# Optimization experiments

Measured on AMD Instinct MI355X. Metric: run time of the kernel, lower is better.

## Reference

```python
import jax, jax.numpy as jnp
import numpy as np

MODES = (16, 16)

def setup_inputs() -> dict:
    key = jax.random.key(0)
    ks = jax.random.split(key, 8)
    B, Cin, Cout, H, W = 16, 64, 64, 128, 128
    scale = 1.0 / (Cin * Cout)
    return {
        "x": jax.random.normal(ks[0], (B, Cin, H, W), jnp.float32),
        "t_emb": jax.random.normal(ks[1], (B, 512), jnp.float32),
        "weight_real": jax.random.normal(ks[2], (Cin, Cout, *MODES), jnp.float32) * 2 * scale - scale,
        "weight_imag": jax.random.normal(ks[3], (Cin, Cout, *MODES), jnp.float32) * 2 * scale - scale,
        "bypass_w": jax.random.normal(ks[4], (Cout, Cin), jnp.float32) * 0.05,
        "bypass_b": jax.random.normal(ks[5], (Cout,), jnp.float32) * 0.05,
        "temb_w": jax.random.normal(ks[6], (Cin, 512), jnp.float32) * 0.02,
        "temb_b": jax.random.normal(ks[7], (Cin,), jnp.float32) * 0.02,
    }

def reference(x, t_emb, weight_real, weight_imag, bypass_w, bypass_b, temb_w, temb_b):
    mk, ml = MODES
    H, W = x.shape[-2:]
    xf = x.astype(jnp.float32)
    # truncated spectral conv: rfft2 (ortho), keep low-mode corner only
    x_fft = jnp.fft.rfftn(xf, axes=(-2, -1), norm="ortho")[:, :, :mk, :ml]
    weight = weight_real + 1j * weight_imag  # [i, o, k, l]
    out_fft = jnp.einsum("bikl,iokl->bokl", x_fft, weight)
    x_spec = jnp.fft.irfftn(out_fft, s=(H, W), axes=(-2, -1), norm="ortho")
    # 1x1 conv bypass
    byp = jnp.einsum("bihw,oi->bohw", xf, bypass_w) + bypass_b[None, :, None, None]
    out = jax.nn.gelu(x_spec + byp, approximate=False)
    # temb fusion: x + Linear(silu(temb))[:, :, None, None]
    silu_t = t_emb * jax.nn.sigmoid(t_emb)
    proj = silu_t @ temb_w.T + temb_b  # [B, C]
    out = out + proj[:, :, None, None]
    return out
```

## Files before the change

kernel.cpp:

```cpp
#include <hip/hip_runtime.h>
#include <cmath>

#define TWO_PI_128 0.04908738521234052f

typedef __attribute__((ext_vector_type(8))) short bf16x8;
typedef __attribute__((ext_vector_type(4))) float f32x4;

__device__ inline unsigned short f2bf(float v) {
  unsigned u = __float_as_uint(v);
  unsigned r = (u + 0x7FFFu + ((u >> 16) & 1u)) >> 16;
  return (unsigned short)r;
}

__global__ __launch_bounds__(256) void front_kernel(
    const float* __restrict__ x, float* __restrict__ xfr_t,
    float* __restrict__ xfi_t, const float* __restrict__ wr,
    const float* __restrict__ wi, float* __restrict__ wt_r,
    float* __restrict__ wt_i, const float* __restrict__ t_emb,
    const float* __restrict__ temb_w, const float* __restrict__ temb_b,
    float* __restrict__ proj) {
  __shared__ union SM {
    struct {
      unsigned short x1[32 * 136];
      float red[8 * 256];
    } f;
    float tile[32][33];
    struct {
      float silu[512];
      float part[64][4];
    } p;
  } sm;

  const int bid = blockIdx.x;
  const int t = threadIdx.x;

  if (bid >= 3072) {
    const int b = bid - 3072;
    for (int j = t; j < 512; j += 256) {
      float v = t_emb[b * 512 + j];
      sm.p.silu[j] = v / (1.f + __expf(-v));
    }
    __syncthreads();
    const int o = t >> 2, part = t & 3;
    const float* wrow = temb_w + o * 512 + part * 128;
    const float* srow = sm.p.silu + part * 128;
    float acc = 0.f;
#pragma unroll 8
    for (int j = 0; j < 128; ++j) acc = fmaf(srow[j], wrow[j], acc);
    sm.p.part[o][part] = acc;
    __syncthreads();
    if (part == 0) {
      proj[b * 64 + o] = sm.p.part[o][0] + sm.p.part[o][1] + sm.p.part[o][2] +
                         sm.p.part[o][3] + temb_b[o];
    }
    return;
  }

  if (bid >= 1024) {
    const int flat = bid - 1024;
    const int tensor = flat >> 10;
    const int rem = flat & 1023;
    const int io0 = (rem >> 3) * 32, kl0 = (rem & 7) * 32;
    const float* src = tensor ? wi : wr;
    float* dst = tensor ? wt_i : wt_r;
    const int ty = t >> 3, tx = t & 7;
    float4 v = *(const float4*)(src + (size_t)(io0 + ty) * 256 + kl0 + 4 * tx);
    sm.tile[ty][4 * tx + 0] = v.x;
    sm.tile[ty][4 * tx + 1] = v.y;
    sm.tile[ty][4 * tx + 2] = v.z;
    sm.tile[ty][4 * tx + 3] = v.w;
    __syncthreads();
    float4 o;
    o.x = sm.tile[4 * tx + 0][ty];
    o.y = sm.tile[4 * tx + 1][ty];
    o.z = sm.tile[4 * tx + 2][ty];
    o.w = sm.tile[4 * tx + 3][ty];
    *(float4*)(dst + (size_t)(kl0 + ty) * 4096 + io0 + 4 * tx) = o;
    return;
  }

  const int plane = bid;
  const int wv = t >> 6, lane = t & 63, l15 = lane & 15, quad = lane >> 4;

  union U8 {
    bf16x8 v;
    unsigned short u[8];
  };

  float dC, dS;
  sincosf(TWO_PI_128 * (float)l15, &dS, &dC);

  U8 a_re[4], a_im[4];
#pragma unroll
  for (int ks = 0; ks < 4; ++ks) {
    const int w0 = ks * 32 + quad * 8;
    float c, s;
    sincosf(TWO_PI_128 * (float)((l15 * w0) & 127), &s, &c);
#pragma unroll
    for (int j = 0; j < 8; ++j) {
      a_re[ks].u[j] = f2bf(c);
      a_im[ks].u[j] = f2bf(-s);
      float nc = c * dC - s * dS;
      s = s * dC + c * dS;
      c = nc;
    }
  }

  const float* xp = x + (size_t)plane * 16384;
  f32x4 acc[2][2];
#pragma unroll
  for (int mt = 0; mt < 2; ++mt)
#pragma unroll
    for (int nt = 0; nt < 2; ++nt) acc[mt][nt] = (f32x4){0.f, 0.f, 0.f, 0.f};

#pragma unroll
  for (int ks = 0; ks < 4; ++ks) {
#pragma unroll
    for (int nt = 0; nt < 2; ++nt) {
      const float* src =
          xp + (size_t)((wv * 2 + nt) * 16 + l15) * 128 + ks * 32 + quad * 8;
      float4 v0 = *(const float4*)src;
      float4 v1 = *(const float4*)(src + 4);
      U8 bx;
      bx.u[0] = f2bf(v0.x);
      bx.u[1] = f2bf(v0.y);
      bx.u[2] = f2bf(v0.z);
      bx.u[3] = f2bf(v0.w);
      bx.u[4] = f2bf(v1.x);
      bx.u[5] = f2bf(v1.y);
      bx.u[6] = f2bf(v1.z);
      bx.u[7] = f2bf(v1.w);
      acc[0][nt] = __builtin_amdgcn_mfma_f32_16x16x32_bf16(a_re[ks].v, bx.v,
                                                           acc[0][nt], 0, 0, 0);
      acc[1][nt] = __builtin_amdgcn_mfma_f32_16x16x32_bf16(a_im[ks].v, bx.v,
                                                           acc[1][nt], 0, 0, 0);
    }
  }

#pragma unroll
  for (int mt = 0; mt < 2; ++mt)
#pragma unroll
    for (int nt = 0; nt < 2; ++nt)
#pragma unroll
      for (int r = 0; r < 4; ++r)
        sm.f.x1[(mt * 16 + quad * 4 + r) * 136 + (wv * 2 + nt) * 16 + l15] =
            f2bf(acc[mt][nt][r]);
  __syncthreads();

  f32x4 accre = (f32x4){0.f, 0.f, 0.f, 0.f};
  f32x4 accim = (f32x4){0.f, 0.f, 0.f, 0.f};
#pragma unroll
  for (int kl2 = 0; kl2 < 2; ++kl2) {
    const int ks2 = wv * 2 + kl2;
    const int hb = (ks2 & 3) * 32 + quad * 8;
    const int imh = ks2 >> 2;
    float c, s;
    sincosf(TWO_PI_128 * (float)((l15 * hb) & 127), &s, &c);
    U8 ar, ai;
#pragma unroll
    for (int j = 0; j < 8; ++j) {
      if (!imh) {
        ar.u[j] = f2bf(c);
        ai.u[j] = f2bf(-s);
      } else {
        ar.u[j] = f2bf(s);
        ai.u[j] = f2bf(c);
      }
      float nc = c * dC - s * dS;
      s = s * dC + c * dS;
      c = nc;
    }
    bf16x8 bfrag = *(const bf16x8*)(sm.f.x1 + (imh * 16 + l15) * 136 + hb);
    accre =
        __builtin_amdgcn_mfma_f32_16x16x32_bf16(ar.v, bfrag, accre, 0, 0, 0);
    accim =
        __builtin_amdgcn_mfma_f32_16x16x32_bf16(ai.v, bfrag, accim, 0, 0, 0);
  }
  *(f32x4*)(sm.f.red + (wv * 2) * 256 + lane * 4) = accre;
  *(f32x4*)(sm.f.red + (wv * 2 + 1) * 256 + lane * 4) = accim;
  __syncthreads();

  const float re =
      sm.f.red[t] + sm.f.red[512 + t] + sm.f.red[1024 + t] + sm.f.red[1536 + t];
  const float im = sm.f.red[256 + t] + sm.f.red[768 + t] + sm.f.red[1280 + t] +
                   sm.f.red[1792 + t];
  const int k = (t >> 6) * 4 + (t & 3), l = (t >> 2) & 15;
  xfr_t[(size_t)(k * 16 + l) * 1024 + plane] = re * 0.0078125f;
  xfi_t[(size_t)(k * 16 + l) * 1024 + plane] = im * 0.0078125f;
}

__global__ __launch_bounds__(1024) void modemix_kernel(
    const float* __restrict__ xfr_t, const float* __restrict__ xfi_t,
    const float* __restrict__ wt_r, const float* __restrict__ wt_i,
    float* __restrict__ ofr, float* __restrict__ ofi) {
  __shared__ float s_xr[1024], s_xi[1024];
  __shared__ float s_wr[4096], s_wi[4096];
  const int kl = blockIdx.x;
  const int t = threadIdx.x;
  if (t < 256)
    ((float4*)s_xr)[t] = ((const float4*)(xfr_t + (size_t)kl * 1024))[t];
  else if (t < 512)
    ((float4*)s_xi)[t - 256] =
        ((const float4*)(xfi_t + (size_t)kl * 1024))[t - 256];
  ((float4*)s_wr)[t] = ((const float4*)(wt_r + (size_t)kl * 4096))[t];
  ((float4*)s_wi)[t] = ((const float4*)(wt_i + (size_t)kl * 4096))[t];
  __syncthreads();
  const int b = t >> 6;
  const int o = t & 63;
  const float* xrp = s_xr + b * 64;
  const float* xip = s_xi + b * 64;
  float ar0 = 0.f, ar1 = 0.f, ai0 = 0.f, ai1 = 0.f;
#pragma unroll 4
  for (int i = 0; i < 64; ++i) {
    float wrv = s_wr[i * 64 + o], wiv = s_wi[i * 64 + o];
    float xr = xrp[i], xi = xip[i];
    ar0 = fmaf(xr, wrv, ar0);
    ar1 = fmaf(xi, wiv, ar1);
    ai0 = fmaf(xr, wiv, ai0);
    ai1 = fmaf(xi, wrv, ai1);
  }
  ofr[(size_t)(b * 64 + o) * 256 + kl] = ar0 - ar1;
  ofi[(size_t)(b * 64 + o) * 256 + kl] = ai0 + ai1;
}

__global__ __launch_bounds__(256) void final_kernel(
    const float* __restrict__ x, const float* __restrict__ bw,
    const float* __restrict__ bb, const float* __restrict__ proj,
    const float* __restrict__ ofr, const float* __restrict__ ofi,
    float* __restrict__ out) {
#define AR 104
  __shared__ unsigned short s_A[64 * AR];
  __shared__ float s_bb[64];
  __shared__ float s_pb[64];
  const int h = blockIdx.x, b = blockIdx.y, t = threadIdx.x;

  if (t < 64)
    s_bb[t] = bb[t];
  else if (t < 128)
    s_pb[t - 64] = proj[b * 64 + (t - 64)];

  {
    const int o = t >> 2, q = t & 3;
    const float4* src = (const float4*)(bw + o * 64 + q * 16);
    unsigned int u[8];
#pragma unroll
    for (int m = 0; m < 4; ++m) {
      float4 v = src[m];
      u[2 * m] = (unsigned)f2bf(v.x) | ((unsigned)f2bf(v.y) << 16);
      u[2 * m + 1] = (unsigned)f2bf(v.z) | ((unsigned)f2bf(v.w) << 16);
    }
    uint4* dst = (uint4*)(s_A + o * AR + q * 16);
    dst[0] = make_uint4(u[0], u[1], u[2], u[3]);
    dst[1] = make_uint4(u[4], u[5], u[6], u[7]);
  }
  {
    const int o = t >> 2, lq = t & 3;
    const float* FR = ofr + (size_t)(b * 64 + o) * 256 + lq * 4;
    const float* FI = ofi + (size_t)(b * 64 + o) * 256 + lq * 4;
    float dS, dC;
    sincosf(TWO_PI_128 * (float)h, &dS, &dC);
    float ck = 1.f, sk = 0.f;
    float yr[4] = {0.f, 0.f, 0.f, 0.f};
    float yi[4] = {0.f, 0.f, 0.f, 0.f};
#pragma unroll 4
    for (int k = 0; k < 16; ++k) {
      float4 fr = *(const float4*)(FR + k * 16);
      float4 fi = *(const float4*)(FI + k * 16);
      yr[0] = fmaf(fr.x, ck, yr[0]);
      yr[0] = fmaf(-fi.x, sk, yr[0]);
      yi[0] = fmaf(fi.x, ck, yi[0]);
      yi[0] = fmaf(fr.x, sk, yi[0]);
      yr[1] = fmaf(fr.y, ck, yr[1]);
      yr[1] = fmaf(-fi.y, sk, yr[1]);
      yi[1] = fmaf(fi.y, ck, yi[1]);
      yi[1] = fmaf(fr.y, sk, yi[1]);
      yr[2] = fmaf(fr.z, ck, yr[2]);
      yr[2] = fmaf(-fi.z, sk, yr[2]);
      yi[2] = fmaf(fi.z, ck, yi[2]);
      yi[2] = fmaf(fr.z, sk, yi[2]);
      yr[3] = fmaf(fr.w, ck, yr[3]);
      yr[3] = fmaf(-fi.w, sk, yr[3]);
      yi[3] = fmaf(fi.w, ck, yi[3]);
      yi[3] = fmaf(fr.w, sk, yi[3]);
      float tt = sk * dS, uu = ck * dS;
      ck = fmaf(ck, dC, -tt);
      sk = fmaf(sk, dC, uu);
    }
    const float scl0 = (lq == 0) ? 0.0078125f : 0.015625f;
    unsigned ur0 = (unsigned)f2bf(yr[0] * scl0) |
                   ((unsigned)f2bf(yr[1] * 0.015625f) << 16);
    unsigned ur1 = (unsigned)f2bf(yr[2] * 0.015625f) |
                   ((unsigned)f2bf(yr[3] * 0.015625f) << 16);
    unsigned ui0 = (unsigned)f2bf(yi[0] * scl0) |
                   ((unsigned)f2bf(yi[1] * 0.015625f) << 16);
    unsigned ui1 = (unsigned)f2bf(yi[2] * 0.015625f) |
                   ((unsigned)f2bf(yi[3] * 0.015625f) << 16);
    *(uint2*)(s_A + o * AR + 64 + lq * 4) = make_uint2(ur0, ur1);
    *(uint2*)(s_A + o * AR + 64 + 16 + lq * 4) = make_uint2(ui0, ui1);
  }
  __syncthreads();

  const int wv = t >> 6, lane = t & 63;
  const int l15 = lane & 15, quad = lane >> 4;
  const int n0w = wv * 32;

  f32x4 acc[4][2];
#pragma unroll
  for (int mt = 0; mt < 4; ++mt) {
    f32x4 bv = *(const f32x4*)(s_bb + mt * 16 + quad * 4);
    acc[mt][0] = bv;
    acc[mt][1] = bv;
  }

  const float* xrow = x + (size_t)b * 1048576 + (size_t)h * 128 + n0w + l15;
#pragma unroll
  for (int ks = 0; ks < 64; ks += 32) {
    union {
      bf16x8 v;
      unsigned short u[8];
    } bx[2];
#pragma unroll
    for (int nt = 0; nt < 2; ++nt) {
      float xv[8];
#pragma unroll
      for (int j = 0; j < 8; ++j)
        xv[j] = xrow[(size_t)(ks + quad * 8 + j) * 16384 + nt * 16];
#pragma unroll
      for (int j = 0; j < 8; ++j) bx[nt].u[j] = f2bf(xv[j]);
    }
#pragma unroll
    for (int mt = 0; mt < 4; ++mt) {
      bf16x8 a = *(const bf16x8*)(s_A + (mt * 16 + l15) * AR + ks + quad * 8);
      acc[mt][0] = __builtin_amdgcn_mfma_f32_16x16x32_bf16(a, bx[0].v,
                                                           acc[mt][0], 0, 0, 0);
      acc[mt][1] = __builtin_amdgcn_mfma_f32_16x16x32_bf16(a, bx[1].v,
                                                           acc[mt][1], 0, 0, 0);
    }
  }

  {
    const int lbase = (quad & 1) * 8;
    const bool iscos = (quad < 2);
    union {
      bf16x8 v;
      unsigned short u[8];
    } bs[2];
#pragma unroll
    for (int nt = 0; nt < 2; ++nt) {
      const int wn = n0w + nt * 16 + l15;
      float st, ct, ss, cc;
      sincosf(TWO_PI_128 * (float)wn, &st, &ct);
      sincosf(TWO_PI_128 * (float)(wn * lbase), &ss, &cc);
#pragma unroll
      for (int j = 0; j < 8; ++j) {
        bs[nt].u[j] = f2bf(iscos ? cc : -ss);
        float nc = cc * ct - ss * st;
        ss = ss * ct + cc * st;
        cc = nc;
      }
    }
#pragma unroll
    for (int mt = 0; mt < 4; ++mt) {
      bf16x8 a = *(const bf16x8*)(s_A + (mt * 16 + l15) * AR + 64 + quad * 8);
      acc[mt][0] = __builtin_amdgcn_mfma_f32_16x16x32_bf16(a, bs[0].v,
                                                           acc[mt][0], 0, 0, 0);
      acc[mt][1] = __builtin_amdgcn_mfma_f32_16x16x32_bf16(a, bs[1].v,
                                                           acc[mt][1], 0, 0, 0);
    }
  }

#pragma unroll
  for (int mt = 0; mt < 4; ++mt) {
    f32x4 pv = *(const f32x4*)(s_pb + mt * 16 + quad * 4);
#pragma unroll
    for (int nt = 0; nt < 2; ++nt) {
      const int wcol = n0w + nt * 16 + l15;
#pragma unroll
      for (int r = 0; r < 4; ++r) {
        const int o = mt * 16 + quad * 4 + r;
        float v = acc[mt][nt][r];
        float g = fmaf(0.5f * v, 1.f + erff(v * 0.70710678f), pv[r]);
        out[((size_t)(b * 64 + o) * 128 + h) * 128 + wcol] = g;
      }
    }
  }
#undef AR
}

extern "C" void kernel_launch(void* const* d_in, const int* in_sizes, int n_in,
                              void* d_out, int out_size, void* d_ws,
                              size_t ws_size, hipStream_t stream) {
  (void)in_sizes;
  (void)n_in;
  (void)out_size;
  (void)ws_size;
  const float* x = (const float*)d_in[0];
  const float* t_emb = (const float*)d_in[1];
  const float* wr = (const float*)d_in[2];
  const float* wi = (const float*)d_in[3];
  const float* bw = (const float*)d_in[4];
  const float* bb = (const float*)d_in[5];
  const float* tw = (const float*)d_in[6];
  const float* tb = (const float*)d_in[7];
  float* out = (float*)d_out;

  char* ws = (char*)d_ws;
  float* proj = (float*)(ws);
  float* ofr = (float*)(ws + ((size_t)1 << 20));
  float* ofi = (float*)(ws + ((size_t)2 << 20));
  float* xfr_t = (float*)(ws + ((size_t)3 << 20));
  float* xfi_t = (float*)(ws + ((size_t)4 << 20));
  float* wt_r = (float*)(ws + ((size_t)5 << 20));
  float* wt_i = (float*)(ws + ((size_t)9 << 20));

  front_kernel<<<3088, 256, 0, stream>>>(x, xfr_t, xfi_t, wr, wi, wt_r, wt_i,
                                         t_emb, tw, tb, proj);
  modemix_kernel<<<256, 1024, 0, stream>>>(xfr_t, xfi_t, wt_r, wt_i, ofr, ofi);
  final_kernel<<<dim3(128, 16), 256, 0, stream>>>(x, bw, bb, proj, ofr, ofi,
                                                  out);
}
```

Before: 169.9 us.

## Precompute twiddle tables in front kernel and prefetch x early in final kernel

An extra block in the front kernel now builds the cos/sin twiddle table for the H-direction inverse DFT and the bf16 spectral B-fragments for the W-direction. The final kernel reads these tables instead of running sincosf and the recurrences per thread. It also loads all 32 x values into registers at kernel start so the global loads overlap the setup work, and it sets a launch bound of 4 blocks per SM. The cost is more register pressure and extra small global reads. The tables are rebuilt on every call, so no state carries over between calls.

```diff
diff --git a/kernel.cpp b/kernel.cpp
--- a/kernel.cpp
+++ b/kernel.cpp
@@ -18,7 +18,8 @@
     const float* __restrict__ wi, float* __restrict__ wt_r,
     float* __restrict__ wt_i, const float* __restrict__ t_emb,
     const float* __restrict__ temb_w, const float* __restrict__ temb_b,
-    float* __restrict__ proj) {
+    float* __restrict__ proj, float2* __restrict__ Tck,
+    unsigned short* __restrict__ Tspec) {
   __shared__ union SM {
     struct {
       unsigned short x1[32 * 136];
@@ -33,6 +34,37 @@
 
   const int bid = blockIdx.x;
   const int t = threadIdx.x;
+
+  if (bid >= 3088) {
+    if (t < 128) {
+      float dS, dC;
+      sincosf(TWO_PI_128 * (float)t, &dS, &dC);
+      float ck = 1.f, sk = 0.f;
+      for (int k = 0; k < 16; ++k) {
+        Tck[t * 16 + k] = make_float2(ck, sk);
+        float tt = sk * dS, uu = ck * dS;
+        ck = fmaf(ck, dC, -tt);
+        sk = fmaf(sk, dC, uu);
+      }
+    } else {
+      const int wn = t - 128;
+      float st, ct;
+      sincosf(TWO_PI_128 * (float)wn, &st, &ct);
+#pragma unroll
+      for (int half = 0; half < 2; ++half) {
+        float ss, cc;
+        sincosf(TWO_PI_128 * (float)(wn * (half * 8)), &ss, &cc);
+        for (int j = 0; j < 8; ++j) {
+          Tspec[wn * 32 + half * 8 + j] = f2bf(cc);
+          Tspec[wn * 32 + 16 + half * 8 + j] = f2bf(-ss);
+          float nc = cc * ct - ss * st;
+          ss = ss * ct + cc * st;
+          cc = nc;
+        }
+      }
+    }
+    return;
+  }
 
   if (bid >= 3072) {
     const int b = bid - 3072;
@@ -223,16 +255,39 @@
   ofi[(size_t)(b * 64 + o) * 256 + kl] = ai0 + ai1;
 }
 
-__global__ __launch_bounds__(256) void final_kernel(
+__global__ __launch_bounds__(256, 4) void final_kernel(
     const float* __restrict__ x, const float* __restrict__ bw,
     const float* __restrict__ bb, const float* __restrict__ proj,
     const float* __restrict__ ofr, const float* __restrict__ ofi,
+    const float2* __restrict__ Tck, const unsigned short* __restrict__ Tspec,
     float* __restrict__ out) {
 #define AR 104
   __shared__ unsigned short s_A[64 * AR];
   __shared__ float s_bb[64];
   __shared__ float s_pb[64];
   const int h = blockIdx.x, b = blockIdx.y, t = threadIdx.x;
+  const int wv = t >> 6, lane = t & 63;
+  const int l15 = lane & 15, quad = lane >> 4;
+  const int n0w = wv * 32;
+
+  float xv[32];
+  {
+    const float* xbase = x + (size_t)b * 1048576 + (size_t)h * 128;
+#pragma unroll
+    for (int ks2 = 0; ks2 < 2; ++ks2)
+#pragma unroll
+      for (int nt = 0; nt < 2; ++nt)
+#pragma unroll
+        for (int j = 0; j < 8; ++j)
+          xv[(ks2 * 2 + nt) * 8 + j] =
+              xbase[(size_t)(ks2 * 32 + quad * 8 + j) * 16384 + n0w + nt * 16 +
+                    l15];
+  }
+
+  bf16x8 tsf[2];
+#pragma unroll
+  for (int nt = 0; nt < 2; ++nt)
+    tsf[nt] = *(const bf16x8*)(Tspec + (n0w + nt * 16 + l15) * 32 + quad * 8);
 
   if (t < 64)
     s_bb[t] = bb[t];
@@ -257,15 +312,15 @@
     const int o = t >> 2, lq = t & 3;
     const float* FR = ofr + (size_t)(b * 64 + o) * 256 + lq * 4;
     const float* FI = ofi + (size_t)(b * 64 + o) * 256 + lq * 4;
-    float dS, dC;
-    sincosf(TWO_PI_128 * (float)h, &dS, &dC);
-    float ck = 1.f, sk = 0.f;
+    const float2* tckrow = Tck + h * 16;
     float yr[4] = {0.f, 0.f, 0.f, 0.f};
     float yi[4] = {0.f, 0.f, 0.f, 0.f};
 #pragma unroll 4
     for (int k = 0; k < 16; ++k) {
       float4 fr = *(const float4*)(FR + k * 16);
       float4 fi = *(const float4*)(FI + k * 16);
+      const float2 cs = tckrow[k];
+      const float ck = cs.x, sk = cs.y;
       yr[0] = fmaf(fr.x, ck, yr[0]);
       yr[0] = fmaf(-fi.x, sk, yr[0]);
       yi[0] = fmaf(fi.x, ck, yi[0]);
@@ -282,9 +337,6 @@
       yr[3] = fmaf(-fi.w, sk, yr[3]);
       yi[3] = fmaf(fi.w, ck, yi[3]);
       yi[3] = fmaf(fr.w, sk, yi[3]);
-      float tt = sk * dS, uu = ck * dS;
-      ck = fmaf(ck, dC, -tt);
-      sk = fmaf(sk, dC, uu);
     }
     const float scl0 = (lq == 0) ? 0.0078125f : 0.015625f;
     unsigned ur0 = (unsigned)f2bf(yr[0] * scl0) |
@@ -300,10 +352,6 @@
   }
   __syncthreads();
 
-  const int wv = t >> 6, lane = t & 63;
-  const int l15 = lane & 15, quad = lane >> 4;
-  const int n0w = wv * 32;
-
   f32x4 acc[4][2];
 #pragma unroll
   for (int mt = 0; mt < 4; ++mt) {
@@ -312,25 +360,21 @@
     acc[mt][1] = bv;
   }
 
-  const float* xrow = x + (size_t)b * 1048576 + (size_t)h * 128 + n0w + l15;
-#pragma unroll
-  for (int ks = 0; ks < 64; ks += 32) {
+#pragma unroll
+  for (int ks2 = 0; ks2 < 2; ++ks2) {
     union {
       bf16x8 v;
       unsigned short u[8];
     } bx[2];
 #pragma unroll
-    for (int nt = 0; nt < 2; ++nt) {
-      float xv[8];
+    for (int nt = 0; nt < 2; ++nt)
 #pragma unroll
       for (int j = 0; j < 8; ++j)
-        xv[j] = xrow[(size_t)(ks + quad * 8 + j) * 16384 + nt * 16];
-#pragma unroll
-      for (int j = 0; j < 8; ++j) bx[nt].u[j] = f2bf(xv[j]);
-    }
+        bx[nt].u[j] = f2bf(xv[(ks2 * 2 + nt) * 8 + j]);
 #pragma unroll
     for (int mt = 0; mt < 4; ++mt) {
-      bf16x8 a = *(const bf16x8*)(s_A + (mt * 16 + l15) * AR + ks + quad * 8);
+      bf16x8 a =
+          *(const bf16x8*)(s_A + (mt * 16 + l15) * AR + ks2 * 32 + quad * 8);
       acc[mt][0] = __builtin_amdgcn_mfma_f32_16x16x32_bf16(a, bx[0].v,
                                                            acc[mt][0], 0, 0, 0);
       acc[mt][1] = __builtin_amdgcn_mfma_f32_16x16x32_bf16(a, bx[1].v,
@@ -338,35 +382,13 @@
     }
   }
 
-  {
-    const int lbase = (quad & 1) * 8;
-    const bool iscos = (quad < 2);
-    union {
-      bf16x8 v;
-      unsigned short u[8];
-    } bs[2];
-#pragma unroll
-    for (int nt = 0; nt < 2; ++nt) {
-      const int wn = n0w + nt * 16 + l15;
-      float st, ct, ss, cc;
-      sincosf(TWO_PI_128 * (float)wn, &st, &ct);
-      sincosf(TWO_PI_128 * (float)(wn * lbase), &ss, &cc);
-#pragma unroll
-      for (int j = 0; j < 8; ++j) {
-        bs[nt].u[j] = f2bf(iscos ? cc : -ss);
-        float nc = cc * ct - ss * st;
-        ss = ss * ct + cc * st;
-        cc = nc;
-      }
-    }
-#pragma unroll
-    for (int mt = 0; mt < 4; ++mt) {
-      bf16x8 a = *(const bf16x8*)(s_A + (mt * 16 + l15) * AR + 64 + quad * 8);
-      acc[mt][0] = __builtin_amdgcn_mfma_f32_16x16x32_bf16(a, bs[0].v,
-                                                           acc[mt][0], 0, 0, 0);
-      acc[mt][1] = __builtin_amdgcn_mfma_f32_16x16x32_bf16(a, bs[1].v,
-                                                           acc[mt][1], 0, 0, 0);
-    }
+#pragma unroll
+  for (int mt = 0; mt < 4; ++mt) {
+    bf16x8 a = *(const bf16x8*)(s_A + (mt * 16 + l15) * AR + 64 + quad * 8);
+    acc[mt][0] =
+        __builtin_amdgcn_mfma_f32_16x16x32_bf16(a, tsf[0], acc[mt][0], 0, 0, 0);
+    acc[mt][1] =
+        __builtin_amdgcn_mfma_f32_16x16x32_bf16(a, tsf[1], acc[mt][1], 0, 0, 0);
   }
 
 #pragma unroll
@@ -412,10 +434,12 @@
   float* xfi_t = (float*)(ws + ((size_t)4 << 20));
   float* wt_r = (float*)(ws + ((size_t)5 << 20));
   float* wt_i = (float*)(ws + ((size_t)9 << 20));
-
-  front_kernel<<<3088, 256, 0, stream>>>(x, xfr_t, xfi_t, wr, wi, wt_r, wt_i,
-                                         t_emb, tw, tb, proj);
+  float2* Tck = (float2*)(ws + ((size_t)13 << 20));
+  unsigned short* Tspec = (unsigned short*)(ws + ((size_t)13 << 20) + 65536);
+
+  front_kernel<<<3089, 256, 0, stream>>>(x, xfr_t, xfi_t, wr, wi, wt_r, wt_i,
+                                         t_emb, tw, tb, proj, Tck, Tspec);
   modemix_kernel<<<256, 1024, 0, stream>>>(xfr_t, xfi_t, wt_r, wt_i, ofr, ofi);
   final_kernel<<<dim3(128, 16), 256, 0, stream>>>(x, bw, bb, proj, ofr, ofi,
-                                                  out);
+                                                  Tck, Tspec, out);
 }
```

Result: no change. 168.4 us (-0.9%).
